# Kernel optimization log

Measured on AMD Instinct MI355X. Metric: run time of the kernel, lower is better.

Reference implementation:

```python
import jax, jax.numpy as jnp
import numpy as np

B, S, HID, NH = 8, 1024, 1024, 16
HD = HID // NH


def setup_inputs() -> dict:
    key = jax.random.key(0)
    ks = jax.random.split(key, 7)
    scale = 1.0 / np.sqrt(HID)
    return {
        "x": jax.random.normal(ks[0], (B, S, HID), dtype=jnp.float32),
        "attention_mask": jax.random.uniform(ks[1], (B, 1, S, S), dtype=jnp.float32),
        "Wq": jax.random.normal(ks[2], (HID, HID), dtype=jnp.float32) * scale,
        "bq": jnp.zeros((HID,), jnp.float32),
        "Wk": jax.random.normal(ks[3], (HID, HID), dtype=jnp.float32) * scale,
        "bk": jnp.zeros((HID,), jnp.float32),
        "Wv": jax.random.normal(ks[4], (HID, HID), dtype=jnp.float32) * scale,
        "bv": jnp.zeros((HID,), jnp.float32),
        "Wp": jax.random.normal(ks[5], (HID, HID), dtype=jnp.float32) * scale,
        "bp": jnp.zeros((HID,), jnp.float32),
    }


def _split(t):
    # [B, S, HID] -> [B, NH, S, HD]
    b, s, _ = t.shape
    return t.reshape(b, s, NH, HD).transpose(0, 2, 1, 3)


def reference(x, attention_mask, Wq, bq, Wk, bk, Wv, bv, Wp, bp):
    q = _split(x @ Wq + bq)  # [B, NH, S, HD]
    k = _split(x @ Wk + bk)
    v = _split(x @ Wv + bv)
    # NOTE: module scales by rsqrt(full hidden_dim) = rsqrt(NH*HD), faithful to source
    scores = jnp.einsum("bhqd,bhkd->bhqk", q, k) * jax.lax.rsqrt(jnp.float32(HID))
    scores = scores + attention_mask * (-1e9)
    attn = jax.nn.softmax(scores, axis=-1)
    ctx = jnp.einsum("bhqk,bhkd->bhqd", attn, v)  # [B, NH, S, HD]
    ctx = ctx.transpose(0, 2, 1, 3).reshape(x.shape[0], x.shape[1], HID)
    # projection (Conv1D k=1 == dense); dropout is identity at inference
    return ctx @ Wp + bp
```

## Files before the change

### kernel.cpp

```cpp
#include <hip/hip_runtime.h>


using bf16x8 = __attribute__((ext_vector_type(8))) short;
using f32x4  = __attribute__((ext_vector_type(4))) float;

#define DEVFN __device__ __forceinline__

typedef const __attribute__((address_space(1))) void gas_void;
typedef __attribute__((address_space(3))) void las_void;

DEVFN void gload16(const void* g, void* l) {
  __builtin_amdgcn_global_load_lds((gas_void*)g, (las_void*)l, 16, 0, 0);
}

DEVFN unsigned short f2bf(float f) {
  union { float f; unsigned u; } v; v.f = f;
  unsigned r = v.u + 0x7fffu + ((v.u >> 16) & 1u);
  return (unsigned short)(r >> 16);
}

__global__ __launch_bounds__(256) void k_convert_x(const float* __restrict__ x,
                                                   unsigned short* __restrict__ xb) {
  int i = (blockIdx.x * 256 + threadIdx.x) * 4;
  float4 v = *reinterpret_cast<const float4*>(x + i);
  ushort4 o;
  o.x = f2bf(v.x); o.y = f2bf(v.y); o.z = f2bf(v.z); o.w = f2bf(v.w);
  *reinterpret_cast<ushort4*>(xb + i) = o;
}

__global__ __launch_bounds__(256) void k_transpose_w(const float* __restrict__ Wq,
                                                     const float* __restrict__ Wk,
                                                     const float* __restrict__ Wv,
                                                     const float* __restrict__ Wp,
                                                     unsigned short* __restrict__ Wcat,
                                                     unsigned short* __restrict__ Wpt) {
  __shared__ float tile[64][65];
  int z = blockIdx.z;
  const float* W = (z == 0) ? Wq : (z == 1) ? Wk : (z == 2) ? Wv : Wp;
  unsigned short* out = (z == 3) ? Wpt : (Wcat + (size_t)z * 1024 * 1024);
  int k0 = blockIdx.y * 64, n0 = blockIdx.x * 64;
  int t = threadIdx.x;
  int tr = t >> 4, tc = (t & 15) * 4;
#pragma unroll
  for (int p = 0; p < 4; ++p) {
    int k = p * 16 + tr;
    float4 v = *reinterpret_cast<const float4*>(W + (size_t)(k0 + k) * 1024 + n0 + tc);
    tile[k][tc + 0] = v.x; tile[k][tc + 1] = v.y;
    tile[k][tc + 2] = v.z; tile[k][tc + 3] = v.w;
  }
  __syncthreads();
#pragma unroll
  for (int p = 0; p < 4; ++p) {
    int n = p * 16 + tr;
    ushort4 o;
    o.x = f2bf(tile[tc + 0][n]); o.y = f2bf(tile[tc + 1][n]);
    o.z = f2bf(tile[tc + 2][n]); o.w = f2bf(tile[tc + 3][n]);
    *reinterpret_cast<ushort4*>(out + (size_t)(n0 + n) * 1024 + k0 + tc) = o;
  }
}

template <int MODE>
__global__ __launch_bounds__(256) void k_gemm(const unsigned short* __restrict__ A,
                                              const unsigned short* __restrict__ Bt,
                                              const float* __restrict__ b0,
                                              const float* __restrict__ b1,
                                              const float* __restrict__ b2,
                                              unsigned short* __restrict__ Qb,
                                              unsigned short* __restrict__ Kb,
                                              unsigned short* __restrict__ Vtb,
                                              float* __restrict__ outp) {
  __shared__ unsigned short As[128 * 64];
  __shared__ unsigned short Bs[128 * 64];
  int t = threadIdx.x, lane = t & 63, w = t >> 6;
  int lgrp = lane >> 4, l16 = lane & 15;
  int n0 = blockIdx.x * 128, m0 = blockIdx.y * 128;
  int wm = w >> 1, wn = w & 1;
  const unsigned short* Ag = A + (size_t)m0 * 1024;
  const unsigned short* Bg = Bt + (size_t)n0 * 1024;

  const f32x4 zf = {0.f, 0.f, 0.f, 0.f};
  f32x4 acc[4][4];
#pragma unroll
  for (int mi = 0; mi < 4; ++mi)
#pragma unroll
    for (int ni = 0; ni < 4; ++ni) acc[mi][ni] = zf;

  for (int kt = 0; kt < 16; ++kt) {
    int kof = kt * 64;
#pragma unroll
    for (int is = 0; is < 4; ++is) {
      int ci = is * 256 + t;
      int row = ci >> 3, c = ci & 7;
      gload16(Ag + (size_t)row * 1024 + kof + c * 8, As + ci * 8);
      gload16(Bg + (size_t)row * 1024 + kof + c * 8, Bs + ci * 8);
    }
    __syncthreads();
    bf16x8 af[4][2], bfr[4][2];
#pragma unroll
    for (int mi = 0; mi < 4; ++mi)
#pragma unroll
      for (int s = 0; s < 2; ++s)
        af[mi][s] = *reinterpret_cast<const bf16x8*>(
            As + (wm * 64 + mi * 16 + l16) * 64 + s * 32 + lgrp * 8);
#pragma unroll
    for (int ni = 0; ni < 4; ++ni)
#pragma unroll
      for (int s = 0; s < 2; ++s)
        bfr[ni][s] = *reinterpret_cast<const bf16x8*>(
            Bs + (wn * 64 + ni * 16 + l16) * 64 + s * 32 + lgrp * 8);
#pragma unroll
    for (int mi = 0; mi < 4; ++mi)
#pragma unroll
      for (int ni = 0; ni < 4; ++ni)
#pragma unroll
        for (int s = 0; s < 2; ++s)
          acc[mi][ni] = __builtin_amdgcn_mfma_f32_16x16x32_bf16(
              af[mi][s], bfr[ni][s], acc[mi][ni], 0, 0, 0);
    __syncthreads();
  }

  if (MODE == 0) {
    int seg = n0 >> 10;
    int nn0 = n0 & 1023;
    const float* bias = (seg == 0) ? b0 : (seg == 1) ? b1 : b2;
#pragma unroll
    for (int ni = 0; ni < 4; ++ni) {
      int nl = wn * 64 + ni * 16 + l16;
      int n = nn0 + nl;
      float bval = bias[n];
#pragma unroll
      for (int mi = 0; mi < 4; ++mi) {
        int ml = wm * 64 + mi * 16 + lgrp * 4;
        if (seg < 2) {
          unsigned short* o = (seg == 0) ? Qb : Kb;
#pragma unroll
          for (int r = 0; r < 4; ++r)
            o[(size_t)(m0 + ml + r) * 1024 + n] = f2bf(acc[mi][ni][r] + bval);
        } else {
          int h = n >> 6, d = n & 63;
          int mg = m0 + ml;
          int bb = mg >> 10, s = mg & 1023;
          ushort4 o4;
          o4.x = f2bf(acc[mi][ni][0] + bval);
          o4.y = f2bf(acc[mi][ni][1] + bval);
          o4.z = f2bf(acc[mi][ni][2] + bval);
          o4.w = f2bf(acc[mi][ni][3] + bval);
          *reinterpret_cast<ushort4*>(Vtb + ((size_t)(bb * 16 + h) * 64 + d) * 1024 + s) = o4;
        }
      }
    }
  } else {
#pragma unroll
    for (int ni = 0; ni < 4; ++ni) {
      int n = n0 + wn * 64 + ni * 16 + l16;
      float bval = b0[n];
#pragma unroll
      for (int mi = 0; mi < 4; ++mi) {
        int ml = wm * 64 + mi * 16 + lgrp * 4;
#pragma unroll
        for (int r = 0; r < 4; ++r)
          outp[(size_t)(m0 + ml + r) * 1024 + n] = acc[mi][ni][r] + bval;
      }
    }
  }
}

__global__ __launch_bounds__(256) void k_attn(const unsigned short* __restrict__ Qb,
                                              const unsigned short* __restrict__ Kb,
                                              const unsigned short* __restrict__ Vtb,
                                              const float* __restrict__ mask,
                                              unsigned short* __restrict__ ctx) {
  __shared__ unsigned short Qs[64 * 64];
  __shared__ unsigned short Ks[64 * 64];
  __shared__ unsigned short Vts[64 * 64];
  __shared__ unsigned short Ps[4][16 * 80];

  int t = threadIdx.x, lane = t & 63, w = t >> 6;
  int lgrp = lane >> 4, l16 = lane & 15;
  int qt = blockIdx.x, bh = blockIdx.y, b = bh >> 4, h = bh & 15;

  {
    const unsigned short* Qg = Qb + ((size_t)(b * 1024 + qt * 64)) * 1024 + h * 64;
#pragma unroll
    for (int is = 0; is < 2; ++is) {
      int ci = is * 256 + t, row = ci >> 3, c = ci & 7, cs = c ^ (row & 7);
      gload16(Qg + (size_t)row * 1024 + cs * 8, Qs + ci * 8);
    }
  }
  __syncthreads();
  bf16x8 aq[2];
  {
    int row = w * 16 + l16;
#pragma unroll
    for (int s = 0; s < 2; ++s) {
      int c = (s * 4 + lgrp) ^ (row & 7);
      aq[s] = *reinterpret_cast<const bf16x8*>(Qs + row * 64 + c * 8);
    }
  }

  const f32x4 zf = {0.f, 0.f, 0.f, 0.f};
  f32x4 acc[4];
#pragma unroll
  for (int dt = 0; dt < 4; ++dt) acc[dt] = zf;
  float m_r[4], l_r[4];
#pragma unroll
  for (int r = 0; r < 4; ++r) { m_r[r] = -__builtin_inff(); l_r[r] = 0.f; }

  const float* mrow = mask + (size_t)b * 1024 * 1024;
  int qg0 = qt * 64 + w * 16 + lgrp * 4;

  for (int kt = 0; kt < 16; ++kt) {
    const unsigned short* Kg = Kb + ((size_t)(b * 1024 + kt * 64)) * 1024 + h * 64;
    const unsigned short* Vg = Vtb + ((size_t)(b * 16 + h) * 64) * 1024 + kt * 64;
#pragma unroll
    for (int is = 0; is < 2; ++is) {
      int ci = is * 256 + t, row = ci >> 3, c = ci & 7, cs = c ^ (row & 7);
      gload16(Kg + (size_t)row * 1024 + cs * 8, Ks + ci * 8);
      gload16(Vg + (size_t)row * 1024 + cs * 8, Vts + ci * 8);
    }
    float mk[4][4];
#pragma unroll
    for (int ct = 0; ct < 4; ++ct)
#pragma unroll
      for (int r = 0; r < 4; ++r)
        mk[ct][r] = mrow[(size_t)(qg0 + r) * 1024 + kt * 64 + ct * 16 + l16];
    __syncthreads();

    f32x4 sac[4];
#pragma unroll
    for (int ct = 0; ct < 4; ++ct) {
      sac[ct] = zf;
#pragma unroll
      for (int s = 0; s < 2; ++s) {
        int row = ct * 16 + l16;
        int c = (s * 4 + lgrp) ^ (row & 7);
        bf16x8 bk_ = *reinterpret_cast<const bf16x8*>(Ks + row * 64 + c * 8);
        sac[ct] = __builtin_amdgcn_mfma_f32_16x16x32_bf16(aq[s], bk_, sac[ct], 0, 0, 0);
      }
    }

    float pv[4][4], rmax[4];
#pragma unroll
    for (int r = 0; r < 4; ++r) {
      float mx = -__builtin_inff();
#pragma unroll
      for (int ct = 0; ct < 4; ++ct) {
        float sc = __fadd_rn(__fmul_rn(sac[ct][r], 0.03125f), __fmul_rn(mk[ct][r], -1e9f));
        pv[ct][r] = sc;
        mx = fmaxf(mx, sc);
      }
#pragma unroll
      for (int off = 1; off < 16; off <<= 1) mx = fmaxf(mx, __shfl_xor(mx, off));
      rmax[r] = mx;
    }
    float resc[4];
#pragma unroll
    for (int r = 0; r < 4; ++r) {
      float mn = fmaxf(m_r[r], rmax[r]);
      resc[r] = __expf(m_r[r] - mn);
      m_r[r] = mn;
    }
#pragma unroll
    for (int r = 0; r < 4; ++r) {
      float rs = 0.f;
#pragma unroll
      for (int ct = 0; ct < 4; ++ct) {
        float p = __expf(pv[ct][r] - m_r[r]);
        pv[ct][r] = p;
        rs += p;
      }
#pragma unroll
      for (int off = 1; off < 16; off <<= 1) rs += __shfl_xor(rs, off);
      l_r[r] = l_r[r] * resc[r] + rs;
    }
#pragma unroll
    for (int dt = 0; dt < 4; ++dt)
#pragma unroll
      for (int r = 0; r < 4; ++r) acc[dt][r] *= resc[r];

#pragma unroll
    for (int ct = 0; ct < 4; ++ct)
#pragma unroll
      for (int r = 0; r < 4; ++r)
        Ps[w][(lgrp * 4 + r) * 80 + ct * 16 + l16] = f2bf(pv[ct][r]);
    asm volatile("" ::: "memory");

#pragma unroll
    for (int s = 0; s < 2; ++s) {
      bf16x8 ap = *reinterpret_cast<const bf16x8*>(&Ps[w][l16 * 80 + s * 32 + lgrp * 8]);
#pragma unroll
      for (int dt = 0; dt < 4; ++dt) {
        int row = dt * 16 + l16;
        int c = (s * 4 + lgrp) ^ (row & 7);
        bf16x8 bv_ = *reinterpret_cast<const bf16x8*>(Vts + row * 64 + c * 8);
        acc[dt] = __builtin_amdgcn_mfma_f32_16x16x32_bf16(ap, bv_, acc[dt], 0, 0, 0);
      }
    }
    __syncthreads();
  }

#pragma unroll
  for (int dt = 0; dt < 4; ++dt)
#pragma unroll
    for (int r = 0; r < 4; ++r) {
      float v = acc[dt][r] / l_r[r];
      size_t m = (size_t)(b * 1024 + qt * 64 + w * 16 + lgrp * 4 + r);
      ctx[m * 1024 + h * 64 + dt * 16 + l16] = f2bf(v);
    }
}

extern "C" void kernel_launch(void* const* d_in, const int* in_sizes, int n_in,
                              void* d_out, int out_size, void* d_ws, size_t ws_size,
                              hipStream_t stream) {
  const float* x    = (const float*)d_in[0];
  const float* mask = (const float*)d_in[1];
  const float* Wq = (const float*)d_in[2];
  const float* bq = (const float*)d_in[3];
  const float* Wk = (const float*)d_in[4];
  const float* bk = (const float*)d_in[5];
  const float* Wv = (const float*)d_in[6];
  const float* bv = (const float*)d_in[7];
  const float* Wp = (const float*)d_in[8];
  const float* bp = (const float*)d_in[9];

  const size_t MB = 1u << 20;
  char* ws = (char*)d_ws;
  unsigned short* xbf  = (unsigned short*)(ws + 0);
  unsigned short* Wcat = (unsigned short*)(ws + 16 * MB);
  unsigned short* Wpt  = (unsigned short*)(ws + 22 * MB);
  unsigned short* Qb   = (unsigned short*)(ws + 24 * MB);
  unsigned short* Kb   = (unsigned short*)(ws + 40 * MB);
  unsigned short* Vtb  = (unsigned short*)(ws + 56 * MB);
  unsigned short* ctx  = xbf;

  k_convert_x<<<8192, 256, 0, stream>>>(x, xbf);
  k_transpose_w<<<dim3(16, 16, 4), 256, 0, stream>>>(Wq, Wk, Wv, Wp, Wcat, Wpt);
  k_gemm<0><<<dim3(24, 64), 256, 0, stream>>>(xbf, Wcat, bq, bk, bv, Qb, Kb, Vtb, nullptr);
  k_attn<<<dim3(16, 128), 256, 0, stream>>>(Qb, Kb, Vtb, mask, ctx);
  k_gemm<1><<<dim3(8, 64), 256, 0, stream>>>(ctx, Wpt, bp, nullptr, nullptr,
                                             nullptr, nullptr, nullptr, (float*)d_out);
}
```

Before: 350.0 us.

## Double-buffer K/V in attention, transpose scores, remap blocks for XCD locality, stage V via LDS

The attention kernel now double-buffers K and V tiles in LDS and prefetches the next mask tile as float4 registers, so loads overlap with compute. It also computes S transposed so each lane owns one query row, which cuts shuffle reductions. The grid is remapped so the 16 heads of the same batch and query tile share an XCD, letting their mask rows reuse cache. P is packed with v_cvt_pk_bf16_f32, and the QKV GEMM's V-transpose store is staged through LDS to produce coalesced 16-byte writes. The cost is more LDS use and more register pressure.

```diff
diff --git a/kernel.cpp b/kernel.cpp
--- a/kernel.cpp
+++ b/kernel.cpp
@@ -17,6 +17,12 @@
   union { float f; unsigned u; } v; v.f = f;
   unsigned r = v.u + 0x7fffu + ((v.u >> 16) & 1u);
   return (unsigned short)(r >> 16);
+}
+
+DEVFN unsigned cvtpk(float lo, float hi) {
+  unsigned r;
+  asm("v_cvt_pk_bf16_f32 %0, %1, %2" : "=v"(r) : "v"(lo), "v"(hi));
+  return r;
 }
 
 __global__ __launch_bounds__(256) void k_convert_x(const float* __restrict__ x,
@@ -69,8 +75,9 @@
                                               unsigned short* __restrict__ Kb,
                                               unsigned short* __restrict__ Vtb,
                                               float* __restrict__ outp) {
-  __shared__ unsigned short As[128 * 64];
-  __shared__ unsigned short Bs[128 * 64];
+  __shared__ unsigned short sm[128 * 128];
+  unsigned short* As = sm;
+  unsigned short* Bs = sm + 128 * 64;
   int t = threadIdx.x, lane = t & 63, w = t >> 6;
   int lgrp = lane >> 4, l16 = lane & 15;
   int n0 = blockIdx.x * 128, m0 = blockIdx.y * 128;
@@ -123,30 +130,45 @@
     int seg = n0 >> 10;
     int nn0 = n0 & 1023;
     const float* bias = (seg == 0) ? b0 : (seg == 1) ? b1 : b2;
-#pragma unroll
-    for (int ni = 0; ni < 4; ++ni) {
-      int nl = wn * 64 + ni * 16 + l16;
-      int n = nn0 + nl;
-      float bval = bias[n];
-#pragma unroll
-      for (int mi = 0; mi < 4; ++mi) {
-        int ml = wm * 64 + mi * 16 + lgrp * 4;
-        if (seg < 2) {
-          unsigned short* o = (seg == 0) ? Qb : Kb;
+    if (seg < 2) {
+      unsigned short* o = (seg == 0) ? Qb : Kb;
+#pragma unroll
+      for (int ni = 0; ni < 4; ++ni) {
+        int n = nn0 + wn * 64 + ni * 16 + l16;
+        float bval = bias[n];
+#pragma unroll
+        for (int mi = 0; mi < 4; ++mi) {
+          int ml = wm * 64 + mi * 16 + lgrp * 4;
 #pragma unroll
           for (int r = 0; r < 4; ++r)
             o[(size_t)(m0 + ml + r) * 1024 + n] = f2bf(acc[mi][ni][r] + bval);
-        } else {
-          int h = n >> 6, d = n & 63;
-          int mg = m0 + ml;
-          int bb = mg >> 10, s = mg & 1023;
-          ushort4 o4;
-          o4.x = f2bf(acc[mi][ni][0] + bval);
-          o4.y = f2bf(acc[mi][ni][1] + bval);
-          o4.z = f2bf(acc[mi][ni][2] + bval);
-          o4.w = f2bf(acc[mi][ni][3] + bval);
-          *reinterpret_cast<ushort4*>(Vtb + ((size_t)(bb * 16 + h) * 64 + d) * 1024 + s) = o4;
         }
+      }
+    } else {
+#pragma unroll
+      for (int ni = 0; ni < 4; ++ni) {
+        int nl = wn * 64 + ni * 16 + l16;
+        float bval = bias[nn0 + nl];
+        int sw = (nl & 7) << 3;
+#pragma unroll
+        for (int mi = 0; mi < 4; ++mi) {
+          int ml = wm * 64 + mi * 16 + lgrp * 4;
+#pragma unroll
+          for (int r = 0; r < 4; ++r)
+            sm[nl * 128 + ((ml + r) ^ sw)] = f2bf(acc[mi][ni][r] + bval);
+        }
+      }
+      __syncthreads();
+      int bb = m0 >> 10, s0 = m0 & 1023;
+      int nl = t >> 1, mh = (t & 1) * 64;
+      int ng = nn0 + nl, hh = ng >> 6, d = ng & 63;
+      unsigned short* vb = Vtb + ((size_t)(bb * 16 + hh) * 64 + d) * 1024 + s0;
+      int sw = (nl & 7) << 3;
+#pragma unroll
+      for (int j = 0; j < 8; ++j) {
+        int me = mh + j * 8;
+        bf16x8 v = *reinterpret_cast<const bf16x8*>(sm + nl * 128 + (me ^ sw));
+        *reinterpret_cast<bf16x8*>(vb + me) = v;
       }
     }
   } else {
@@ -171,23 +193,36 @@
                                               const float* __restrict__ mask,
                                               unsigned short* __restrict__ ctx) {
   __shared__ unsigned short Qs[64 * 64];
-  __shared__ unsigned short Ks[64 * 64];
-  __shared__ unsigned short Vts[64 * 64];
-  __shared__ unsigned short Ps[4][16 * 80];
+  __shared__ unsigned short Ks[2][64 * 64];
+  __shared__ unsigned short Vts[2][64 * 64];
+  __shared__ unsigned short Ps[4][16 * 72];
 
   int t = threadIdx.x, lane = t & 63, w = t >> 6;
   int lgrp = lane >> 4, l16 = lane & 15;
-  int qt = blockIdx.x, bh = blockIdx.y, b = bh >> 4, h = bh & 15;
-
-  {
-    const unsigned short* Qg = Qb + ((size_t)(b * 1024 + qt * 64)) * 1024 + h * 64;
-#pragma unroll
-    for (int is = 0; is < 2; ++is) {
-      int ci = is * 256 + t, row = ci >> 3, c = ci & 7, cs = c ^ (row & 7);
-      gload16(Qg + (size_t)row * 1024 + cs * 8, Qs + ci * 8);
-    }
-  }
+  int gid = blockIdx.x;
+  int xcd = gid & 7, ii = gid >> 3;
+  int grp = (ii >> 4) * 8 + xcd;
+  int h = ii & 15;
+  int b = grp >> 4, qt = grp & 15;
+
+  const unsigned short* Qg = Qb + ((size_t)(b * 1024 + qt * 64)) * 1024 + h * 64;
+  const unsigned short* Kg = Kb + (size_t)b * 1024 * 1024 + h * 64;
+  const unsigned short* Vg = Vtb + ((size_t)(b * 16 + h) * 64) * 1024;
+  const float* mrow = mask + (size_t)b * 1024 * 1024 + (size_t)(qt * 64 + w * 16 + l16) * 1024;
+
+#pragma unroll
+  for (int is = 0; is < 2; ++is) {
+    int ci = is * 256 + t, row = ci >> 3, c = ci & 7, cs = c ^ (row & 7);
+    gload16(Qg + (size_t)row * 1024 + cs * 8, Qs + ci * 8);
+    gload16(Kg + (size_t)row * 1024 + cs * 8, Ks[0] + ci * 8);
+    gload16(Vg + (size_t)row * 1024 + cs * 8, Vts[0] + ci * 8);
+  }
+  float4 mkc[4], mkn[4];
+#pragma unroll
+  for (int ct = 0; ct < 4; ++ct)
+    mkc[ct] = *reinterpret_cast<const float4*>(mrow + ct * 16 + lgrp * 4);
   __syncthreads();
+
   bf16x8 aq[2];
   {
     int row = w * 16 + l16;
@@ -202,111 +237,102 @@
   f32x4 acc[4];
 #pragma unroll
   for (int dt = 0; dt < 4; ++dt) acc[dt] = zf;
-  float m_r[4], l_r[4];
-#pragma unroll
-  for (int r = 0; r < 4; ++r) { m_r[r] = -__builtin_inff(); l_r[r] = 0.f; }
-
-  const float* mrow = mask + (size_t)b * 1024 * 1024;
-  int qg0 = qt * 64 + w * 16 + lgrp * 4;
+  float m_s = -__builtin_inff(), l_s = 0.f;
+  int cur = 0;
 
   for (int kt = 0; kt < 16; ++kt) {
-    const unsigned short* Kg = Kb + ((size_t)(b * 1024 + kt * 64)) * 1024 + h * 64;
-    const unsigned short* Vg = Vtb + ((size_t)(b * 16 + h) * 64) * 1024 + kt * 64;
-#pragma unroll
-    for (int is = 0; is < 2; ++is) {
-      int ci = is * 256 + t, row = ci >> 3, c = ci & 7, cs = c ^ (row & 7);
-      gload16(Kg + (size_t)row * 1024 + cs * 8, Ks + ci * 8);
-      gload16(Vg + (size_t)row * 1024 + cs * 8, Vts + ci * 8);
-    }
-    float mk[4][4];
-#pragma unroll
-    for (int ct = 0; ct < 4; ++ct)
-#pragma unroll
-      for (int r = 0; r < 4; ++r)
-        mk[ct][r] = mrow[(size_t)(qg0 + r) * 1024 + kt * 64 + ct * 16 + l16];
-    __syncthreads();
-
-    f32x4 sac[4];
+    if (kt < 15) {
+#pragma unroll
+      for (int is = 0; is < 2; ++is) {
+        int ci = is * 256 + t, row = ci >> 3, c = ci & 7, cs = c ^ (row & 7);
+        gload16(Kg + (size_t)(kt + 1) * 64 * 1024 + (size_t)row * 1024 + cs * 8,
+                Ks[cur ^ 1] + ci * 8);
+        gload16(Vg + (size_t)row * 1024 + (kt + 1) * 64 + cs * 8, Vts[cur ^ 1] + ci * 8);
+      }
+#pragma unroll
+      for (int ct = 0; ct < 4; ++ct)
+        mkn[ct] = *reinterpret_cast<const float4*>(mrow + (kt + 1) * 64 + ct * 16 + lgrp * 4);
+    }
+
+    float sc[16];
+    float mx = -__builtin_inff();
 #pragma unroll
     for (int ct = 0; ct < 4; ++ct) {
-      sac[ct] = zf;
+      f32x4 sac = zf;
 #pragma unroll
       for (int s = 0; s < 2; ++s) {
         int row = ct * 16 + l16;
         int c = (s * 4 + lgrp) ^ (row & 7);
-        bf16x8 bk_ = *reinterpret_cast<const bf16x8*>(Ks + row * 64 + c * 8);
-        sac[ct] = __builtin_amdgcn_mfma_f32_16x16x32_bf16(aq[s], bk_, sac[ct], 0, 0, 0);
-      }
-    }
-
-    float pv[4][4], rmax[4];
-#pragma unroll
-    for (int r = 0; r < 4; ++r) {
-      float mx = -__builtin_inff();
-#pragma unroll
-      for (int ct = 0; ct < 4; ++ct) {
-        float sc = __fadd_rn(__fmul_rn(sac[ct][r], 0.03125f), __fmul_rn(mk[ct][r], -1e9f));
-        pv[ct][r] = sc;
-        mx = fmaxf(mx, sc);
-      }
-#pragma unroll
-      for (int off = 1; off < 16; off <<= 1) mx = fmaxf(mx, __shfl_xor(mx, off));
-      rmax[r] = mx;
-    }
-    float resc[4];
-#pragma unroll
-    for (int r = 0; r < 4; ++r) {
-      float mn = fmaxf(m_r[r], rmax[r]);
-      resc[r] = __expf(m_r[r] - mn);
-      m_r[r] = mn;
-    }
-#pragma unroll
-    for (int r = 0; r < 4; ++r) {
-      float rs = 0.f;
-#pragma unroll
-      for (int ct = 0; ct < 4; ++ct) {
-        float p = __expf(pv[ct][r] - m_r[r]);
-        pv[ct][r] = p;
-        rs += p;
-      }
-#pragma unroll
-      for (int off = 1; off < 16; off <<= 1) rs += __shfl_xor(rs, off);
-      l_r[r] = l_r[r] * resc[r] + rs;
-    }
+        bf16x8 ak = *reinterpret_cast<const bf16x8*>(Ks[cur] + row * 64 + c * 8);
+        sac = __builtin_amdgcn_mfma_f32_16x16x32_bf16(ak, aq[s], sac, 0, 0, 0);
+      }
+      const float* mp = reinterpret_cast<const float*>(&mkc[ct]);
+#pragma unroll
+      for (int r = 0; r < 4; ++r) {
+        float v = __fadd_rn(__fmul_rn(sac[r], 0.03125f), __fmul_rn(mp[r], -1e9f));
+        sc[ct * 4 + r] = v;
+        mx = fmaxf(mx, v);
+      }
+    }
+    mx = fmaxf(mx, __shfl_xor(mx, 16, 64));
+    mx = fmaxf(mx, __shfl_xor(mx, 32, 64));
+    float mn = fmaxf(m_s, mx);
+    float resc = __expf(m_s - mn);
+    m_s = mn;
+    float rs = 0.f;
+#pragma unroll
+    for (int i = 0; i < 16; ++i) {
+      float p = __expf(sc[i] - mn);
+      sc[i] = p;
+      rs += p;
+    }
+    rs += __shfl_xor(rs, 16, 64);
+    rs += __shfl_xor(rs, 32, 64);
+    l_s = l_s * resc + rs;
+
+    float racc[4];
+#pragma unroll
+    for (int r = 0; r < 4; ++r) racc[r] = __shfl(resc, lgrp * 4 + r, 64);
 #pragma unroll
     for (int dt = 0; dt < 4; ++dt)
 #pragma unroll
-      for (int r = 0; r < 4; ++r) acc[dt][r] *= resc[r];
-
-#pragma unroll
-    for (int ct = 0; ct < 4; ++ct)
-#pragma unroll
-      for (int r = 0; r < 4; ++r)
-        Ps[w][(lgrp * 4 + r) * 80 + ct * 16 + l16] = f2bf(pv[ct][r]);
+      for (int r = 0; r < 4; ++r) acc[dt][r] *= racc[r];
+
+#pragma unroll
+    for (int ct = 0; ct < 4; ++ct) {
+      uint2 u;
+      u.x = cvtpk(sc[ct * 4 + 0], sc[ct * 4 + 1]);
+      u.y = cvtpk(sc[ct * 4 + 2], sc[ct * 4 + 3]);
+      *reinterpret_cast<uint2*>(&Ps[w][l16 * 72 + ct * 16 + lgrp * 4]) = u;
+    }
     asm volatile("" ::: "memory");
 
 #pragma unroll
     for (int s = 0; s < 2; ++s) {
-      bf16x8 ap = *reinterpret_cast<const bf16x8*>(&Ps[w][l16 * 80 + s * 32 + lgrp * 8]);
+      bf16x8 ap = *reinterpret_cast<const bf16x8*>(&Ps[w][l16 * 72 + s * 32 + lgrp * 8]);
 #pragma unroll
       for (int dt = 0; dt < 4; ++dt) {
         int row = dt * 16 + l16;
         int c = (s * 4 + lgrp) ^ (row & 7);
-        bf16x8 bv_ = *reinterpret_cast<const bf16x8*>(Vts + row * 64 + c * 8);
+        bf16x8 bv_ = *reinterpret_cast<const bf16x8*>(Vts[cur] + row * 64 + c * 8);
         acc[dt] = __builtin_amdgcn_mfma_f32_16x16x32_bf16(ap, bv_, acc[dt], 0, 0, 0);
       }
     }
     __syncthreads();
-  }
-
+    cur ^= 1;
+#pragma unroll
+    for (int ct = 0; ct < 4; ++ct) mkc[ct] = mkn[ct];
+  }
+
+  float linv[4];
+#pragma unroll
+  for (int r = 0; r < 4; ++r) linv[r] = 1.0f / __shfl(l_s, lgrp * 4 + r, 64);
+  size_t mbase = (size_t)(b * 1024 + qt * 64 + w * 16 + lgrp * 4);
 #pragma unroll
   for (int dt = 0; dt < 4; ++dt)
 #pragma unroll
-    for (int r = 0; r < 4; ++r) {
-      float v = acc[dt][r] / l_r[r];
-      size_t m = (size_t)(b * 1024 + qt * 64 + w * 16 + lgrp * 4 + r);
-      ctx[m * 1024 + h * 64 + dt * 16 + l16] = f2bf(v);
-    }
+    for (int r = 0; r < 4; ++r)
+      ctx[(mbase + r) * 1024 + h * 64 + dt * 16 + l16] = f2bf(acc[dt][r] * linv[r]);
 }
 
 extern "C" void kernel_launch(void* const* d_in, const int* in_sizes, int n_in,
@@ -336,7 +362,7 @@
   k_convert_x<<<8192, 256, 0, stream>>>(x, xbf);
   k_transpose_w<<<dim3(16, 16, 4), 256, 0, stream>>>(Wq, Wk, Wv, Wp, Wcat, Wpt);
   k_gemm<0><<<dim3(24, 64), 256, 0, stream>>>(xbf, Wcat, bq, bk, bv, Qb, Kb, Vtb, nullptr);
-  k_attn<<<dim3(16, 128), 256, 0, stream>>>(Qb, Kb, Vtb, mask, ctx);
+  k_attn<<<2048, 256, 0, stream>>>(Qb, Kb, Vtb, mask, ctx);
   k_gemm<1><<<dim3(8, 64), 256, 0, stream>>>(ctx, Wpt, bp, nullptr, nullptr,
                                              nullptr, nullptr, nullptr, (float*)d_out);
 }
```

New measurement: 342.0 us. -2.3%, faster.
